# Optimization experiments

Measured on AMD Instinct MI355X. Metric: run time of the kernel, lower is better.

The kernel has to match this reference:

```python
import jax, jax.numpy as jnp
import numpy as np

PH, PW = 2, 2
SCALE = (0.5, 0.5)
HARDNESS = 2.0
BN_EPS = 1e-5

def conv2d(x, w, b, pad):
    y = jax.lax.conv_general_dilated(x, w, (1, 1), [(pad, pad), (pad, pad)],
                                     dimension_numbers=('NCHW', 'OIHW', 'NCHW'))
    return y + b[None, :, None, None]

def nearest_resize(x, oh, ow):
    # torch F.interpolate default 'nearest': src_idx = floor(dst_idx * in/out)
    _, _, ih, iw = x.shape
    hi = jnp.floor(jnp.arange(oh) * (ih / oh)).astype(jnp.int32)
    wi = jnp.floor(jnp.arange(ow) * (iw / ow)).astype(jnp.int32)
    return x[:, :, hi][:, :, :, wi]

def bilinear_resize(x, oh, ow):
    # matches torch bilinear align_corners=False (half-pixel, no antialias)
    b, c = x.shape[0], x.shape[1]
    return jax.image.resize(x, (b, c, oh, ow), method='linear', antialias=False)

def grid_sample_bilinear(feat, grid):
    # feat [B,C,H,W], grid [B,gh,gw,2] with (x,y) in [-1,1]; align_corners=False, zeros padding
    B, C, H, W = feat.shape
    gx, gy = grid[..., 0], grid[..., 1]
    ix = (gx + 1.0) * (W * 0.5) - 0.5
    iy = (gy + 1.0) * (H * 0.5) - 0.5
    x0f = jnp.floor(ix); y0f = jnp.floor(iy)
    wx = ix - x0f; wy = iy - y0f
    x0 = x0f.astype(jnp.int32); y0 = y0f.astype(jnp.int32)
    x1 = x0 + 1; y1 = y0 + 1

    def gather(f, yy, xx):
        valid = ((yy >= 0) & (yy < H) & (xx >= 0) & (xx < W)).astype(f.dtype)
        yc = jnp.clip(yy, 0, H - 1); xc = jnp.clip(xx, 0, W - 1)
        return f[:, yc, xc] * valid[None]  # [C,gh,gw]

    def per_sample(f, y0, x0, y1, x1, wx, wy):
        v00 = gather(f, y0, x0); v01 = gather(f, y0, x1)
        v10 = gather(f, y1, x0); v11 = gather(f, y1, x1)
        wx_ = wx[None]; wy_ = wy[None]
        return (v00 * (1 - wx_) * (1 - wy_) + v01 * wx_ * (1 - wy_)
                + v10 * (1 - wx_) * wy_ + v11 * wx_ * wy_)

    return jax.vmap(per_sample)(feat, y0, x0, y1, x1, wx, wy)

def lens_forward(feat, w1, b1, gamma, beta, rmean, rvar, w2, b2):
    B, C, H, W = feat.shape
    dh, dw = H // PH, W // PW
    dsz_h, dsz_w = int(H * SCALE[0]), int(W * SCALE[1])
    # ekern: conv3x3 + BN(eval) + ReLU6
    x = conv2d(feat, w1, b1, 1)
    inv = jax.lax.rsqrt(rvar + BN_EPS)
    x = (x - rmean[None, :, None, None]) * inv[None, :, None, None]
    x = x * gamma[None, :, None, None] + beta[None, :, None, None]
    x = jnp.clip(x, 0.0, 6.0)
    # dkern (eval branch): channel-norm normalize with gating, conv5x5 (no pad) + sigmoid
    nrm = jnp.linalg.norm(x, axis=1, keepdims=True)
    xn = x / (nrm + 9e-8) * (nrm > 0.09).astype(x.dtype)
    dmap_raw = jax.nn.sigmoid(conv2d(xn, w2, b2, 0))  # [B,2,H-4,W-4]
    ndmap = nearest_resize(dmap_raw, dh + 2, dw + 2)
    # dmap += 0.0009; interior += hardness
    mask = jnp.zeros((dh + 2, dw + 2), x.dtype).at[1:-1, 1:-1].set(1.0)
    dmap = ndmap + 0.0009 + HARDNESS * mask[None, None]
    # bilinear round trip through dsz
    dsm = bilinear_resize(dmap, dsz_h, dsz_w)
    dmap = bilinear_resize(dsm, dh + 2, dw + 2)
    # neko_dense_norm: normalize, cumsum -> CDF sampling grid in [-1,1]
    h_ = dmap[:, 0:1]; w_ = dmap[:, 1:2]
    h_ = h_ / jnp.sum(h_, axis=2, keepdims=True)
    w_ = w_ / jnp.sum(w_, axis=3, keepdims=True)
    hc = jnp.cumsum(h_, axis=2); wc = jnp.cumsum(w_, axis=3)
    grid = jnp.concatenate([wc[:, :, 1:-1, 1:-1], hc[:, :, 1:-1, 1:-1]], axis=1) * 2 - 1
    grid = jnp.transpose(grid, (0, 2, 3, 1))  # [B,dh,dw,2] (x,y)
    dst = grid_sample_bilinear(feat, grid)  # [B,C,dh,dw]
    # adaptive_avg_pool2d([dh,dw]) on a [dh,dw] map is identity -> skip
    return dst, dmap

def setup_inputs() -> dict:
    key = jax.random.key(0)
    ks = jax.random.split(key, 9)
    B, ICH, H, W, CH = 16, 64, 256, 256, 64
    feat = jax.random.normal(ks[0], (B, ICH, H, W), jnp.float32)
    w1 = jax.random.normal(ks[1], (CH, ICH, 3, 3), jnp.float32) * 0.05
    b1 = jax.random.normal(ks[2], (CH,), jnp.float32) * 0.05
    gamma = 1.0 + jax.random.normal(ks[3], (CH,), jnp.float32) * 0.05
    beta = jax.random.normal(ks[4], (CH,), jnp.float32) * 0.05
    rmean = jax.random.normal(ks[5], (CH,), jnp.float32) * 0.05
    rvar = jax.random.uniform(ks[6], (CH,), jnp.float32) + 0.5
    w2 = jax.random.normal(ks[7], (2, CH, 5, 5), jnp.float32) * 0.05
    b2 = jax.random.normal(ks[8], (2,), jnp.float32) * 0.05
    return {'feat': feat, 'w1': w1, 'b1': b1, 'gamma': gamma, 'beta': beta,
            'rmean': rmean, 'rvar': rvar, 'w2': w2, 'b2': b2}

def reference(feat, w1, b1, gamma, beta, rmean, rvar, w2, b2):
    dst, dmap = lens_forward(feat, w1, b1, gamma, beta, rmean, rvar, w2, b2)
    return dst, jax.lax.stop_gradient(dmap)
```

## Files before the change

kernel.cpp:

```cpp
#include <hip/hip_runtime.h>
#include <hip/hip_bf16.h>

typedef __hip_bfloat16 bf16;
typedef __attribute__((ext_vector_type(8))) short bf16x8;
typedef __attribute__((ext_vector_type(4))) float f32x4;

static __device__ __forceinline__ ushort f2bf(float f) {
    uint u = __float_as_uint(f);
    u += 0x7fff + ((u >> 16) & 1);
    return (ushort)(u >> 16);
}

static __device__ __forceinline__ void gl_lds16(const void* g, void* l) {
    __builtin_amdgcn_global_load_lds(
        (const __attribute__((address_space(1))) uint*)g,
        (__attribute__((address_space(3))) uint*)l, 16, 0, 0);
}

static __device__ __forceinline__ int xcd_remap(int lid, int nwg) {
    int q = nwg >> 3, r = nwg & 7;
    int xcd = lid & 7, idx = lid >> 3;
    return (xcd < r ? xcd * (q + 1) : r * (q + 1) + (xcd - r) * q) + idx;
}

#define FT_ROW 264
#define FT_IMG ((size_t)258 * 264 * 64)
#define XN_IMG ((size_t)256 * 256 * 64)

__global__ __launch_bounds__(256) void k_prep(const float* __restrict__ w1,
                                              const float* __restrict__ w2,
                                              ushort* __restrict__ w_bf,
                                              ushort* __restrict__ w2_bf,
                                              ushort* __restrict__ featT, int nb) {
    int i = blockIdx.x * 256 + threadIdx.x;
    if (i < 36864) {
        int oc = i / 576, rem = i - oc * 576;
        int ic = rem / 9, tap = rem - ic * 9;
        w_bf[tap * 4096 + oc * 64 + (ic ^ ((oc & 7) << 3))] = f2bf(w1[i]);
    } else if (i < 40064) {
        int j = i - 36864;
        int oc = j / 1600, rem = j - oc * 1600;
        int ic = rem / 25, tap = rem - ic * 25;
        w2_bf[(tap * 2 + oc) * 64 + ic] = f2bf(w2[j]);
    } else {
        int t = i - 40064;
        const int per = 1040 * 8;
        if (t >= nb * per) return;
        int b = t / per, u = t - b * per;
        int px = u >> 3, oct = u & 7;
        int yp, xp;
        if (px < 264)       { yp = 0;   xp = px; }
        else if (px < 528)  { yp = 257; xp = px - 264; }
        else { int k = px - 528; yp = 1 + (k >> 1); xp = (k & 1) ? 257 : 0; }
        ushort* p = featT + (size_t)b * FT_IMG + ((size_t)yp * FT_ROW + xp) * 64 + oct * 8;
        *(uint4*)p = make_uint4(0u, 0u, 0u, 0u);
    }
}

__global__ __launch_bounds__(256) void k_tr(const float* __restrict__ feat_c,
                                            ushort* __restrict__ featT) {
    __shared__ ushort s_t[64][72];
    const int b = blockIdx.z, y = blockIdx.y, x0 = blockIdx.x * 64;
    const int t = threadIdx.x;
    const int xl = t & 63, icg = t >> 6;

    const float* fb = feat_c + (size_t)b * 64 * 65536 + (size_t)y * 256 + x0 + xl;
#pragma unroll
    for (int k = 0; k < 16; ++k) {
        int ic = icg * 16 + k;
        s_t[ic][xl] = f2bf(fb[(size_t)ic * 65536]);
    }
    __syncthreads();

    ushort* ob = featT + (size_t)b * FT_IMG + ((size_t)(y + 1) * FT_ROW + (x0 + 1)) * 64;
#pragma unroll
    for (int u2 = 0; u2 < 2; ++u2) {
        int u = u2 * 256 + t;
        int x = u >> 3, oct = u & 7;
        int xp7 = (x + 1) & 7;
        uint p0 = (uint)s_t[oct * 8 + 0][x] | ((uint)s_t[oct * 8 + 1][x] << 16);
        uint p1 = (uint)s_t[oct * 8 + 2][x] | ((uint)s_t[oct * 8 + 3][x] << 16);
        uint p2 = (uint)s_t[oct * 8 + 4][x] | ((uint)s_t[oct * 8 + 5][x] << 16);
        uint p3 = (uint)s_t[oct * 8 + 6][x] | ((uint)s_t[oct * 8 + 7][x] << 16);
        *(uint4*)(ob + (size_t)x * 64 + (oct ^ xp7) * 8) = make_uint4(p0, p1, p2, p3);
    }
}

__global__ __launch_bounds__(256, 2) void k_conv1(
    const ushort* __restrict__ featT, const ushort* __restrict__ w_bf,
    const float* __restrict__ b1, const float* __restrict__ gamma,
    const float* __restrict__ beta, const float* __restrict__ rmean,
    const float* __restrict__ rvar, ushort* __restrict__ xn) {
    __shared__ __align__(16) ushort s_in[6 * 72 * 64];
    __shared__ __align__(16) ushort s_w[12288];
    __shared__ float2 s_bn[64];

    const int lid = blockIdx.x + (blockIdx.y << 2) + (blockIdx.z << 8);
    const int nid = xcd_remap(lid, (int)gridDim.z << 8);
    const int b   = nid >> 8;
    const int x0p = (nid & 3) * 64;
    const int y0  = ((nid >> 2) & 63) * 4;

    const int tid = threadIdx.x;
    const int lane = tid & 63;
    const int w    = tid >> 6;
    const int l15  = lane & 15;
    const int l4   = lane >> 4;

    if (tid < 64) {
        float inv = 1.0f / sqrtf(rvar[tid] + 1e-5f);
        float sA = inv * gamma[tid];
        float sB = (b1[tid] - rmean[tid]) * sA + beta[tid];
        s_bn[tid] = make_float2(sA, sB);
    }

    const ushort* fT = featT + (size_t)b * FT_IMG;
    {
        int aStart = w * 13 + (w < 2 ? w : 2);
        int aCnt   = (w < 2) ? 14 : 13;
        for (int q = 0; q < aCnt; ++q) {
            int o = (aStart + q) * 1024;
            int r = o / 9216;
            int rem = o - r * 9216;
            const ushort* g = fT + ((size_t)(y0 + r) * FT_ROW + x0p) * 64 +
                              (rem >> 1) + lane * 8;
            gl_lds16(g, (char*)s_in + o);
        }
    }

    f32x4 acc[4][4];
#pragma unroll
    for (int m = 0; m < 4; m++)
#pragma unroll
        for (int n = 0; n < 4; n++) acc[m][n] = (f32x4){0.f, 0.f, 0.f, 0.f};

    for (int dy = 0; dy < 3; dy++) {
        __syncthreads();
        {
            for (int q = 0; q < 6; ++q) {
                int o = (w * 6 + q) * 1024;
                const ushort* g = w_bf + dy * 12288 + (o >> 1) + lane * 8;
                gl_lds16(g, (char*)s_w + o);
            }
        }
        __syncthreads();
#pragma unroll
        for (int dx = 0; dx < 3; dx++) {
#pragma unroll
            for (int ks = 0; ks < 2; ks++) {
                bf16x8 a[4], bb[4];
#pragma unroll
                for (int m = 0; m < 4; m++) {
                    int c = m * 16 + l15 + dx;
                    int slot = (ks * 4 + l4) ^ (c & 7);
                    a[m] = *(const bf16x8*)&s_in[((w + dy) * 72 + c) * 64 + slot * 8];
                }
#pragma unroll
                for (int n = 0; n < 4; n++) {
                    int oc = n * 16 + l15;
                    int slot = (ks * 4 + l4) ^ (oc & 7);
                    bb[n] = *(const bf16x8*)&s_w[(dx * 64 + oc) * 64 + slot * 8];
                }
#pragma unroll
                for (int m = 0; m < 4; m++)
#pragma unroll
                    for (int n = 0; n < 4; n++)
                        acc[m][n] = __builtin_amdgcn_mfma_f32_16x16x32_bf16(
                            bb[n], a[m], acc[m][n], 0, 0, 0);
            }
        }
    }

    float sA[4][4], sB[4][4];
#pragma unroll
    for (int n = 0; n < 4; n++)
#pragma unroll
        for (int j = 0; j < 4; j++) {
            float2 t = s_bn[n * 16 + l4 * 4 + j];
            sA[n][j] = t.x; sB[n][j] = t.y;
        }
    const int y = y0 + w;
    ushort* xb = xn + (size_t)b * XN_IMG;

#pragma unroll
    for (int m = 0; m < 4; m++) {
        float vv[4][4];
        float ss = 0.f;
#pragma unroll
        for (int n = 0; n < 4; n++)
#pragma unroll
            for (int j = 0; j < 4; j++) {
                float v = fmaf(acc[m][n][j], sA[n][j], sB[n][j]);
                v = fminf(fmaxf(v, 0.f), 6.f);
                vv[n][j] = v;
                ss = fmaf(v, v, ss);
            }
        ss += __shfl_xor(ss, 16);
        ss += __shfl_xor(ss, 32);
        float nrm = sqrtf(ss);
        float sc = (nrm > 0.09f) ? (1.0f / (nrm + 9e-8f)) : 0.f;

        int x = x0p + m * 16 + l15;
        ushort* pb = xb + ((size_t)y * 256 + x) * 64;
        int so = (l4 & 1) * 4;
#pragma unroll
        for (int n = 0; n < 4; n++) {
            int oct = n * 2 + (l4 >> 1);
            int slot = oct ^ (x & 7);
            uint2 pk;
            pk.x = (uint)f2bf(vv[n][0] * sc) | ((uint)f2bf(vv[n][1] * sc) << 16);
            pk.y = (uint)f2bf(vv[n][2] * sc) | ((uint)f2bf(vv[n][3] * sc) << 16);
            *(uint2*)(pb + slot * 8 + so) = pk;
        }
    }
}

__global__ __launch_bounds__(256, 2) void k_conv2(
    const ushort* __restrict__ xn, const ushort* __restrict__ w2_bf,
    const float* __restrict__ b2, float* __restrict__ dmap_raw2) {
    __shared__ __align__(16) ushort s_in[11 * 80 * 32];

    const int lid = blockIdx.x + (blockIdx.y << 2) + blockIdx.z * 132;
    const int nid = xcd_remap(lid, (int)gridDim.z * 132);
    const int b   = nid / 132;
    const int rem = nid - b * 132;
    const int x0  = (rem & 3) * 64;
    const int oy0 = (rem >> 2) * 4;

    const int tid = threadIdx.x;
    const int lane = tid & 63;
    const int w    = tid >> 6;
    const int l15  = lane & 15;
    const int l4   = lane >> 4;

    const float SC = (float)(252.0 / 130.0);
    const int syb = (int)floorf((float)oy0 * SC);
    const int oy  = oy0 + w;
    const int syrel = (int)floorf((float)oy * SC) - syb;

    const ushort* xb = xn + (size_t)b * XN_IMG;

    f32x4 acc[4];
#pragma unroll
    for (int n = 0; n < 4; n++) acc[n] = (f32x4){0.f, 0.f, 0.f, 0.f};

    for (int c = 0; c < 2; ++c) {
        if (c) __syncthreads();
        {
            int st  = (w < 3) ? w * 14 : 42;
            int cnt = (w < 3) ? 14 : 13;
            for (int q = 0; q < cnt; ++q) {
                int i = st + q;
                int r = i / 5;
                int px0 = (i - r * 5) * 16;
                int gr = min(syb + r, 255);
                int px = px0 + (lane >> 2);
                int gx = x0 + px;
                const ushort* g = xb + (size_t)(gr * 256 + gx) * 64 +
                                  ((((gx >> 2) & 1) ^ c) * 32) + (lane & 3) * 8;
                gl_lds16(g, (char*)s_in + i * 1024);
            }
        }
        __syncthreads();

#pragma unroll
        for (int dy = 0; dy < 5; dy++) {
#pragma unroll
            for (int dx = 0; dx < 5; dx++) {
                bf16x8 aw;
                if (l15 < 2)
                    aw = *(const bf16x8*)(w2_bf + ((dy * 5 + dx) * 2 + l15) * 64 +
                                          c * 32 + l4 * 8);
                else
                    aw = (bf16x8){0, 0, 0, 0, 0, 0, 0, 0};
                bf16x8 bx[4];
#pragma unroll
                for (int n = 0; n < 4; n++) {
                    int px = n * 16 + l15 + dx;
                    int slot4 = l4 ^ (px & 3);
                    bx[n] = *(const bf16x8*)&s_in[((syrel + dy) * 80 + px) * 32 + slot4 * 8];
                }
#pragma unroll
                for (int n = 0; n < 4; n++)
                    acc[n] = __builtin_amdgcn_mfma_f32_16x16x32_bf16(
                        aw, bx[n], acc[n], 0, 0, 0);
            }
        }
    }

    if (l4 == 0 && oy < 130) {
        float bias0 = b2[0], bias1 = b2[1];
#pragma unroll
        for (int n = 0; n < 4; n++) {
            int ox = x0 + n * 16 + l15;
            if (ox < 252) {
                float v0 = acc[n][0] + bias0;
                float v1 = acc[n][1] + bias1;
                size_t o = (size_t)b * 65520 + (size_t)oy * 252 + ox;
                dmap_raw2[o] = 1.f / (1.f + expf(-v0));
                dmap_raw2[o + 32760] = 1.f / (1.f + expf(-v1));
            }
        }
    }
}

__global__ __launch_bounds__(256) void k_dmap(const float* __restrict__ dmap_raw2,
                                              float* __restrict__ out_dmap,
                                              float* __restrict__ grid) {
    __shared__ float sA[16900];
    __shared__ float sB[16384];
    const int ch = blockIdx.x, b = blockIdx.y;
    const int tid = threadIdx.x;
    const float SC = (float)(252.0 / 130.0);

    const float* src = dmap_raw2 + (size_t)b * 65520 + (size_t)ch * 32760;
    for (int i = tid; i < 16900; i += 256) {
        int oy = i / 130, ox = i - oy * 130;
        int sx = (int)floorf((float)ox * SC);
        float m = (oy >= 1 && oy <= 128 && ox >= 1 && ox <= 128) ? 2.0f : 0.0f;
        sA[i] = src[oy * 252 + sx] + 0.0009f + m;
    }
    __syncthreads();

    {
        const float sc = (float)(130.0 / 128.0);
        for (int i = tid; i < 16384; i += 256) {
            int oy = i >> 7, ox = i & 127;
            float sy = ((float)oy + 0.5f) * sc - 0.5f;
            float sx = ((float)ox + 0.5f) * sc - 0.5f;
            float y0f = floorf(sy), x0f = floorf(sx);
            float wy = sy - y0f, wx = sx - x0f;
            int y0 = max(min((int)y0f, 129), 0), y1 = max(min((int)y0f + 1, 129), 0);
            int x0 = max(min((int)x0f, 129), 0), x1 = max(min((int)x0f + 1, 129), 0);
            float top = sA[y0 * 130 + x0] * (1.f - wx) + sA[y0 * 130 + x1] * wx;
            float bot = sA[y1 * 130 + x0] * (1.f - wx) + sA[y1 * 130 + x1] * wx;
            sB[i] = top * (1.f - wy) + bot * wy;
        }
    }
    __syncthreads();

    {
        const float sc = (float)(128.0 / 130.0);
        float* od = out_dmap + ((size_t)b * 2 + ch) * 16900;
        for (int i = tid; i < 16900; i += 256) {
            int oy = i / 130, ox = i - oy * 130;
            float sy = ((float)oy + 0.5f) * sc - 0.5f;
            float sx = ((float)ox + 0.5f) * sc - 0.5f;
            float y0f = floorf(sy), x0f = floorf(sx);
            float wy = sy - y0f, wx = sx - x0f;
            int y0 = max(min((int)y0f, 127), 0), y1 = max(min((int)y0f + 1, 127), 0);
            int x0 = max(min((int)x0f, 127), 0), x1 = max(min((int)x0f + 1, 127), 0);
            float top = sB[y0 * 128 + x0] * (1.f - wx) + sB[y0 * 128 + x1] * wx;
            float bot = sB[y1 * 128 + x0] * (1.f - wx) + sB[y1 * 128 + x1] * wx;
            float v = top * (1.f - wy) + bot * wy;
            od[i] = v;
            sA[i] = v;
        }
    }
    __syncthreads();

    if (tid < 130) {
        float* g = grid + (size_t)b * 32768;
        if (ch == 0) {
            float s = 0.f;
            for (int r = 0; r < 130; r++) s += sA[r * 130 + tid];
            float inv = 1.f / s;
            float cs = 0.f;
            for (int r = 0; r < 130; r++) {
                cs += sA[r * 130 + tid] * inv;
                if (r >= 1 && r <= 128 && tid >= 1 && tid <= 128)
                    g[((r - 1) * 128 + (tid - 1)) * 2 + 1] = cs * 2.f - 1.f;
            }
        } else {
            const float* row = sA + tid * 130;
            float s = 0.f;
            for (int x = 0; x < 130; x++) s += row[x];
            float inv = 1.f / s;
            float cs = 0.f;
            for (int x = 0; x < 130; x++) {
                cs += row[x] * inv;
                if (x >= 1 && x <= 128 && tid >= 1 && tid <= 128)
                    g[((tid - 1) * 128 + (x - 1)) * 2 + 0] = cs * 2.f - 1.f;
            }
        }
    }
}

__global__ __launch_bounds__(256) void k_sample(const float* __restrict__ feat_c,
                                                const float* __restrict__ grid,
                                                float* __restrict__ dst_c) {
    const int lid = blockIdx.x + (blockIdx.y << 3) + (blockIdx.z << 6);
    const int nid = xcd_remap(lid, (int)gridDim.z << 6);
    const int b = nid >> 6;
    const int x = ((nid & 7) << 4) + (threadIdx.x & 15);
    const int y = (((nid >> 3) & 7) << 4) + (threadIdx.x >> 4);

    const float* g = grid + (((size_t)b * 128 + y) * 128 + x) * 2;
    float gx = g[0], gy = g[1];
    float ix = (gx + 1.f) * 128.f - 0.5f;
    float iy = (gy + 1.f) * 128.f - 0.5f;
    float x0f = floorf(ix), y0f = floorf(iy);
    float wx = ix - x0f, wy = iy - y0f;
    int ix0 = (int)x0f, iy0 = (int)y0f;
    int ix1 = ix0 + 1, iy1 = iy0 + 1;
    float vx0 = ((unsigned)ix0 < 256u) ? 1.f : 0.f;
    float vx1 = ((unsigned)ix1 < 256u) ? 1.f : 0.f;
    float vy0 = ((unsigned)iy0 < 256u) ? 1.f : 0.f;
    float vy1 = ((unsigned)iy1 < 256u) ? 1.f : 0.f;
    int cx0 = max(min(ix0, 255), 0), cx1 = max(min(ix1, 255), 0);
    int cy0 = max(min(iy0, 255), 0), cy1 = max(min(iy1, 255), 0);
    float w00 = (1.f - wx) * (1.f - wy) * vx0 * vy0;
    float w01 = wx * (1.f - wy) * vx1 * vy0;
    float w10 = (1.f - wx) * wy * vx0 * vy1;
    float w11 = wx * wy * vx1 * vy1;

    const float* fb = feat_c + (size_t)b * 64 * 65536;
    int o00 = cy0 * 256 + cx0, o01 = cy0 * 256 + cx1;
    int o10 = cy1 * 256 + cx0, o11 = cy1 * 256 + cx1;
    float* d = dst_c + (size_t)b * 64 * 16384 + (size_t)y * 128 + x;
#pragma unroll 4
    for (int c = 0; c < 64; c++) {
        const float* fc = fb + (size_t)c * 65536;
        d[(size_t)c * 16384] = fc[o00] * w00 + fc[o01] * w01 +
                               fc[o10] * w10 + fc[o11] * w11;
    }
}

static inline size_t align256(size_t x) { return (x + 255) & ~(size_t)255; }

extern "C" void kernel_launch(void* const* d_in, const int* in_sizes, int n_in,
                              void* d_out, int out_size, void* d_ws, size_t ws_size,
                              hipStream_t stream) {
    const float* feat  = (const float*)d_in[0];
    const float* w1    = (const float*)d_in[1];
    const float* b1    = (const float*)d_in[2];
    const float* gamma = (const float*)d_in[3];
    const float* beta  = (const float*)d_in[4];
    const float* rmean = (const float*)d_in[5];
    const float* rvar  = (const float*)d_in[6];
    const float* w2    = (const float*)d_in[7];
    const float* b2    = (const float*)d_in[8];

    float* out = (float*)d_out;
    float* out_dst  = out;
    float* out_dmap = out + 16777216;

    int nb = 1;
    const int cands[5] = {16, 8, 4, 2, 1};
    for (int k = 0; k < 5; ++k) {
        int n = cands[k];
        size_t need = align256((size_t)n * FT_IMG * 2)
                    + align256((size_t)n * XN_IMG * 2)
                    + align256(73728)
                    + align256(12800)
                    + align256((size_t)n * 65520 * 4)
                    + align256((size_t)n * 131072);
        if (need <= ws_size) { nb = n; break; }
    }

    char* p = (char*)d_ws;
    ushort* featT    = (ushort*)p; p += align256((size_t)nb * FT_IMG * 2);
    ushort* xn       = (ushort*)p; p += align256((size_t)nb * XN_IMG * 2);
    ushort* w_bf     = (ushort*)p; p += align256(73728);
    ushort* w2_bf    = (ushort*)p; p += align256(12800);
    float* dmap_raw2 = (float*)p;  p += align256((size_t)nb * 65520 * 4);
    float* grid      = (float*)p;

    k_prep<<<(40064 + nb * 8320 + 255) / 256, 256, 0, stream>>>(
        w1, w2, w_bf, w2_bf, featT, nb);

    const int nchunks = 16 / nb;
    for (int c = 0; c < nchunks; ++c) {
        const float* feat_c = feat + (size_t)c * nb * 64 * 65536;
        float* dst_c  = out_dst  + (size_t)c * nb * 64 * 16384;
        float* dmap_c = out_dmap + (size_t)c * nb * 2 * 16900;

        k_tr<<<dim3(4, 256, nb), 256, 0, stream>>>(feat_c, featT);
        k_conv1<<<dim3(4, 64, nb), 256, 0, stream>>>(featT, w_bf, b1, gamma,
                                                     beta, rmean, rvar, xn);
        k_conv2<<<dim3(4, 33, nb), 256, 0, stream>>>(xn, w2_bf, b2, dmap_raw2);
        k_dmap<<<dim3(2, nb), 256, 0, stream>>>(dmap_raw2, dmap_c, grid);
        k_sample<<<dim3(8, 8, nb), 256, 0, stream>>>(feat_c, grid, dst_c);
    }
}
```

Baseline: 400.9 us.

## Split conv1 input channels into two halves to halve LDS and raise occupancy

The 3x3 conv kernel now processes the 64 input channels in two 32-channel chunks. Per chunk it stages half the input tile and half of each weight row into LDS, so the LDS footprint halves and launch bounds can go from 2 to 4 blocks per CU. Weight and transposed-feature layouts get a new XOR swizzle that matches 32-channel rows. In exchange there are more barriers and input reloads per block, and the extra occupancy has to hide that added synchronization.

```diff
diff --git a/kernel.cpp b/kernel.cpp
--- a/kernel.cpp
+++ b/kernel.cpp
@@ -36,7 +36,9 @@
     if (i < 36864) {
         int oc = i / 576, rem = i - oc * 576;
         int ic = rem / 9, tap = rem - ic * 9;
-        w_bf[tap * 4096 + oc * 64 + (ic ^ ((oc & 7) << 3))] = f2bf(w1[i]);
+        int c = ic >> 5, icl = ic & 31;
+        int s4 = (icl >> 3) ^ ((oc ^ (oc >> 2)) & 3);
+        w_bf[((c * 9 + tap) * 64 + oc) * 32 + s4 * 8 + (icl & 7)] = f2bf(w1[i]);
     } else if (i < 40064) {
         int j = i - 36864;
         int oc = j / 1600, rem = j - oc * 1600;
@@ -77,22 +79,23 @@
     for (int u2 = 0; u2 < 2; ++u2) {
         int u = u2 * 256 + t;
         int x = u >> 3, oct = u & 7;
-        int xp7 = (x + 1) & 7;
+        int xx = x + 1;
+        int g = (xx ^ (xx >> 2)) & 7;
         uint p0 = (uint)s_t[oct * 8 + 0][x] | ((uint)s_t[oct * 8 + 1][x] << 16);
         uint p1 = (uint)s_t[oct * 8 + 2][x] | ((uint)s_t[oct * 8 + 3][x] << 16);
         uint p2 = (uint)s_t[oct * 8 + 4][x] | ((uint)s_t[oct * 8 + 5][x] << 16);
         uint p3 = (uint)s_t[oct * 8 + 6][x] | ((uint)s_t[oct * 8 + 7][x] << 16);
-        *(uint4*)(ob + (size_t)x * 64 + (oct ^ xp7) * 8) = make_uint4(p0, p1, p2, p3);
-    }
-}
-
-__global__ __launch_bounds__(256, 2) void k_conv1(
+        *(uint4*)(ob + (size_t)x * 64 + (oct ^ g) * 8) = make_uint4(p0, p1, p2, p3);
+    }
+}
+
+__global__ __launch_bounds__(256, 4) void k_conv1(
     const ushort* __restrict__ featT, const ushort* __restrict__ w_bf,
     const float* __restrict__ b1, const float* __restrict__ gamma,
     const float* __restrict__ beta, const float* __restrict__ rmean,
     const float* __restrict__ rvar, ushort* __restrict__ xn) {
-    __shared__ __align__(16) ushort s_in[6 * 72 * 64];
-    __shared__ __align__(16) ushort s_w[12288];
+    __shared__ __align__(16) ushort s_in[6 * 72 * 32];
+    __shared__ __align__(16) ushort s_w[6144];
     __shared__ float2 s_bn[64];
 
     const int lid = blockIdx.x + (blockIdx.y << 2) + (blockIdx.z << 8);
@@ -115,18 +118,6 @@
     }
 
     const ushort* fT = featT + (size_t)b * FT_IMG;
-    {
-        int aStart = w * 13 + (w < 2 ? w : 2);
-        int aCnt   = (w < 2) ? 14 : 13;
-        for (int q = 0; q < aCnt; ++q) {
-            int o = (aStart + q) * 1024;
-            int r = o / 9216;
-            int rem = o - r * 9216;
-            const ushort* g = fT + ((size_t)(y0 + r) * FT_ROW + x0p) * 64 +
-                              (rem >> 1) + lane * 8;
-            gl_lds16(g, (char*)s_in + o);
-        }
-    }
 
     f32x4 acc[4][4];
 #pragma unroll
@@ -134,32 +125,44 @@
 #pragma unroll
         for (int n = 0; n < 4; n++) acc[m][n] = (f32x4){0.f, 0.f, 0.f, 0.f};
 
-    for (int dy = 0; dy < 3; dy++) {
-        __syncthreads();
+    for (int c = 0; c < 2; ++c) {
+        if (c) __syncthreads();
         {
-            for (int q = 0; q < 6; ++q) {
-                int o = (w * 6 + q) * 1024;
-                const ushort* g = w_bf + dy * 12288 + (o >> 1) + lane * 8;
-                gl_lds16(g, (char*)s_w + o);
-            }
-        }
-        __syncthreads();
-#pragma unroll
-        for (int dx = 0; dx < 3; dx++) {
-#pragma unroll
-            for (int ks = 0; ks < 2; ks++) {
+            int st  = (w < 2) ? w * 8 : 16 + (w - 2) * 7;
+            int cnt = (w < 2) ? 8 : 7;
+            for (int q = 0; q < cnt; ++q) {
+                int i = st + q;
+                int r = i / 5, o = i - r * 5;
+                int px0 = (o < 4) ? o * 16 : 56;
+                int px = px0 + (lane >> 2);
+                int h = c ^ (((px >> 2) ^ (px >> 4)) & 1);
+                const ushort* g = fT + ((size_t)(y0 + r) * FT_ROW + x0p + px) * 64 +
+                                  h * 32 + (lane & 3) * 8;
+                gl_lds16(g, (char*)s_in + r * 4608 + px0 * 64);
+            }
+        }
+        for (int dy = 0; dy < 3; ++dy) {
+            __syncthreads();
+            for (int q = 0; q < 3; ++q) {
+                int j = w * 3 + q;
+                const ushort* g = w_bf + (c * 9 + dy * 3) * 2048 + j * 512 + lane * 8;
+                gl_lds16(g, (char*)s_w + j * 1024);
+            }
+            __syncthreads();
+#pragma unroll
+            for (int dx = 0; dx < 3; dx++) {
                 bf16x8 a[4], bb[4];
 #pragma unroll
                 for (int m = 0; m < 4; m++) {
-                    int c = m * 16 + l15 + dx;
-                    int slot = (ks * 4 + l4) ^ (c & 7);
-                    a[m] = *(const bf16x8*)&s_in[((w + dy) * 72 + c) * 64 + slot * 8];
+                    int col = m * 16 + l15 + dx;
+                    int s4 = l4 ^ ((col ^ (col >> 2)) & 3);
+                    a[m] = *(const bf16x8*)&s_in[((w + dy) * 72 + col) * 32 + s4 * 8];
                 }
 #pragma unroll
                 for (int n = 0; n < 4; n++) {
                     int oc = n * 16 + l15;
-                    int slot = (ks * 4 + l4) ^ (oc & 7);
-                    bb[n] = *(const bf16x8*)&s_w[(dx * 64 + oc) * 64 + slot * 8];
+                    int s4 = l4 ^ ((oc ^ (oc >> 2)) & 3);
+                    bb[n] = *(const bf16x8*)&s_w[(dx * 64 + oc) * 32 + s4 * 8];
                 }
 #pragma unroll
                 for (int m = 0; m < 4; m++)
```

Result: slower. 455.4 us (+13.6%).
